# Kernel tuning notes

Measured on AMD Instinct MI355X. Metric: run time of the kernel, lower is better.

Reference implementation:

```python
import jax, jax.numpy as jnp
import numpy as np

FEATURE_SIZE = 1_000_000
CROSS_EMB = 16
NNZ = 819_200
BATCH = 16_384
NEG_SAMPLING_RATE = 1.0


def setup_inputs() -> dict:
    key = jax.random.key(0)
    k_ids, k_seg, k_lw, k_cw, k_b = jax.random.split(key, 5)
    ids = jax.random.randint(k_ids, (NNZ,), 0, FEATURE_SIZE, dtype=jnp.int64 if jax.config.jax_enable_x64 else jnp.int32).astype(jnp.int32)
    segment_ids = jnp.sort(jax.random.randint(k_seg, (NNZ,), 0, BATCH, dtype=jnp.int32))
    linear_bias = jax.random.normal(k_b, (1,), dtype=jnp.float32) * 1e-4
    linear_w = jax.random.normal(k_lw, (FEATURE_SIZE, 1), dtype=jnp.float32) * 1e-4
    cross_emb_w = jax.random.normal(k_cw, (FEATURE_SIZE, CROSS_EMB), dtype=jnp.float32) * 1e-4
    return {
        "ids": ids,
        "segment_ids": segment_ids,
        "batch_size": BATCH,
        "linear_bias": linear_bias,
        "linear_w": linear_w,
        "cross_emb_w": cross_emb_w,
    }


def reference(ids, segment_ids, batch_size, linear_bias, linear_w, cross_emb_w):
    # Embedding-bag (sum combiner) == segment_sum of gathered rows.
    # Partitioned-shard routing in the original is mathematically a single
    # global gather + segment_sum (shard partial sums add up to the same).
    lin_rows = linear_w[ids]                        # [N, 1]
    logits_wide = jax.ops.segment_sum(lin_rows, segment_ids, num_segments=batch_size)  # [B, 1]
    logits_linear = linear_bias + logits_wide

    cross_rows = cross_emb_w[ids]                   # [N, D]
    summed = jax.ops.segment_sum(cross_rows, segment_ids, num_segments=batch_size)     # [B, D]
    squared_summed = jnp.square(summed)
    summed_squared = jax.ops.segment_sum(jnp.square(cross_rows), segment_ids, num_segments=batch_size)
    # FM second-order interaction term
    logits_cross = 0.5 * jnp.sum(squared_summed - summed_squared, axis=1, keepdims=True)  # [B, 1]

    logits = logits_linear + logits_cross
    logits_adjusted = logits + jnp.log(jnp.float32(NEG_SAMPLING_RATE))
    probabilities = jax.nn.sigmoid(logits_adjusted)
    return (logits, logits_adjusted, probabilities)
```

## Files before the change

### kernel.cpp

```cpp
#include <hip/hip_runtime.h>
#include <math.h>


__global__ __launch_bounds__(256) void seg_starts_kernel(
    const int* __restrict__ segs, int* __restrict__ starts, int nnz, int batch)
{
    const int i = blockIdx.x * blockDim.x + threadIdx.x;
    if (i >= nnz) return;
    const int cur = segs[i];
    if (i == 0) {
        for (int b = 0; b <= cur; ++b) starts[b] = 0;
    } else {
        const int prev = segs[i - 1];
        for (int b = prev + 1; b <= cur; ++b) starts[b] = i;
    }
    if (i == nnz - 1) {
        for (int b = cur + 1; b <= batch; ++b) starts[b] = nnz;
    }
}

__global__ __launch_bounds__(256) void fm_fused_kernel(
    const int* __restrict__ ids,
    const int* __restrict__ starts,
    const float* __restrict__ bias,
    const float* __restrict__ lw,
    const float* __restrict__ cw,
    float* __restrict__ out,
    int batch)
{
    const int wave = threadIdx.x >> 6;
    const int wl   = threadIdx.x & 63;
    const int b    = blockIdx.x * 4 + wave;
    if (b >= batch) return;

    const int start = starts[b];
    const int end   = starts[b + 1];

    float sd[16];
    #pragma unroll
    for (int d = 0; d < 16; ++d) sd[d] = 0.f;
    float ssq = 0.f;
    float slin = 0.f;

    for (int i = start + wl; i < end; i += 64) {
        const int id = ids[i];
        const float* row = cw + ((size_t)id << 4);
        const float4 x0 = *reinterpret_cast<const float4*>(row);
        const float4 x1 = *reinterpret_cast<const float4*>(row + 4);
        const float4 x2 = *reinterpret_cast<const float4*>(row + 8);
        const float4 x3 = *reinterpret_cast<const float4*>(row + 12);
        slin += lw[id];
        sd[ 0] += x0.x; sd[ 1] += x0.y; sd[ 2] += x0.z; sd[ 3] += x0.w;
        sd[ 4] += x1.x; sd[ 5] += x1.y; sd[ 6] += x1.z; sd[ 7] += x1.w;
        sd[ 8] += x2.x; sd[ 9] += x2.y; sd[10] += x2.z; sd[11] += x2.w;
        sd[12] += x3.x; sd[13] += x3.y; sd[14] += x3.z; sd[15] += x3.w;
        ssq = fmaf(x0.x, x0.x, ssq); ssq = fmaf(x0.y, x0.y, ssq);
        ssq = fmaf(x0.z, x0.z, ssq); ssq = fmaf(x0.w, x0.w, ssq);
        ssq = fmaf(x1.x, x1.x, ssq); ssq = fmaf(x1.y, x1.y, ssq);
        ssq = fmaf(x1.z, x1.z, ssq); ssq = fmaf(x1.w, x1.w, ssq);
        ssq = fmaf(x2.x, x2.x, ssq); ssq = fmaf(x2.y, x2.y, ssq);
        ssq = fmaf(x2.z, x2.z, ssq); ssq = fmaf(x2.w, x2.w, ssq);
        ssq = fmaf(x3.x, x3.x, ssq); ssq = fmaf(x3.y, x3.y, ssq);
        ssq = fmaf(x3.w, x3.w, ssq); ssq = fmaf(x3.z, x3.z, ssq);
    }

    #pragma unroll
    for (int m = 1; m < 64; m <<= 1) {
        #pragma unroll
        for (int d = 0; d < 16; ++d) sd[d] += __shfl_xor(sd[d], m);
        ssq  += __shfl_xor(ssq,  m);
        slin += __shfl_xor(slin, m);
    }

    if (wl == 0) {
        float q = 0.f;
        #pragma unroll
        for (int d = 0; d < 16; ++d) q = fmaf(sd[d], sd[d], q);
        const float logit = bias[0] + slin + 0.5f * (q - ssq);
        const float adj   = logit;
        out[b]             = logit;
        out[batch + b]     = adj;
        out[2 * batch + b] = 1.0f / (1.0f + expf(-adj));
    }
}

extern "C" void kernel_launch(void* const* d_in, const int* in_sizes, int n_in,
                              void* d_out, int out_size, void* d_ws, size_t ws_size,
                              hipStream_t stream) {
    const int*   ids  = (const int*)d_in[0];
    const int*   segs = (const int*)d_in[1];
    const float* bias = (const float*)d_in[3];
    const float* lw   = (const float*)d_in[4];
    const float* cw   = (const float*)d_in[5];
    float*       out  = (float*)d_out;

    const int nnz   = in_sizes[0];
    const int batch = out_size / 3;

    int* starts = (int*)d_ws;

    seg_starts_kernel<<<(nnz + 255) / 256, 256, 0, stream>>>(segs, starts, nnz, batch);

    const int waves_per_block = 4;
    const int grid = (batch + waves_per_block - 1) / waves_per_block;
    fm_fused_kernel<<<grid, 256, 0, stream>>>(ids, starts, bias, lw, cw, out, batch);
}
```

Measured before the change: 125.0 us.

## Replace per-segment wave reduction with per-nnz segmented scan and atomics

Replaces the segment-starts plus one-wave-per-bag design with a thread-per-nonzero gather. A segmented inclusive scan using shuffle-up combines rows within a wave, and segment tails atomically add 18 partial sums into a zeroed workspace. A separate epilogue kernel then computes the logits and sigmoid. The goal is to avoid the load imbalance and idle lanes of waves assigned to short bags (about 50 nnz per bag across 64 lanes). In exchange it adds a third kernel launch, a workspace zero pass, global atomics, and 18 values times 6 shuffle steps per thread.

New measurement: 142.4 us. +13.9%, slower.

```diff
diff --git a/kernel.cpp b/kernel.cpp
--- a/kernel.cpp
+++ b/kernel.cpp
@@ -2,86 +2,86 @@
 #include <math.h>
 
 
-__global__ __launch_bounds__(256) void seg_starts_kernel(
-    const int* __restrict__ segs, int* __restrict__ starts, int nnz, int batch)
+#define WS_STRIDE 18
+
+__global__ __launch_bounds__(256) void zero_ws_kernel(float* __restrict__ ws, int n)
 {
-    const int i = blockIdx.x * blockDim.x + threadIdx.x;
-    if (i >= nnz) return;
-    const int cur = segs[i];
-    if (i == 0) {
-        for (int b = 0; b <= cur; ++b) starts[b] = 0;
-    } else {
-        const int prev = segs[i - 1];
-        for (int b = prev + 1; b <= cur; ++b) starts[b] = i;
-    }
-    if (i == nnz - 1) {
-        for (int b = cur + 1; b <= batch; ++b) starts[b] = nnz;
-    }
+    const int i = blockIdx.x * 256 + threadIdx.x;
+    if (i < n) ws[i] = 0.f;
 }
 
-__global__ __launch_bounds__(256) void fm_fused_kernel(
+__global__ __launch_bounds__(256) void fm_gather_kernel(
     const int* __restrict__ ids,
-    const int* __restrict__ starts,
-    const float* __restrict__ bias,
+    const int* __restrict__ segs,
     const float* __restrict__ lw,
     const float* __restrict__ cw,
-    float* __restrict__ out,
-    int batch)
+    float* __restrict__ ws,
+    int nnz)
 {
-    const int wave = threadIdx.x >> 6;
-    const int wl   = threadIdx.x & 63;
-    const int b    = blockIdx.x * 4 + wave;
-    if (b >= batch) return;
+    const int i    = blockIdx.x * 256 + threadIdx.x;
+    const int lane = threadIdx.x & 63;
 
-    const int start = starts[b];
-    const int end   = starts[b + 1];
+    int seg = -1;
+    float v[18];
+    #pragma unroll
+    for (int d = 0; d < 18; ++d) v[d] = 0.f;
 
-    float sd[16];
-    #pragma unroll
-    for (int d = 0; d < 16; ++d) sd[d] = 0.f;
-    float ssq = 0.f;
-    float slin = 0.f;
-
-    for (int i = start + wl; i < end; i += 64) {
+    if (i < nnz) {
+        seg = segs[i];
         const int id = ids[i];
         const float* row = cw + ((size_t)id << 4);
         const float4 x0 = *reinterpret_cast<const float4*>(row);
         const float4 x1 = *reinterpret_cast<const float4*>(row + 4);
         const float4 x2 = *reinterpret_cast<const float4*>(row + 8);
         const float4 x3 = *reinterpret_cast<const float4*>(row + 12);
-        slin += lw[id];
-        sd[ 0] += x0.x; sd[ 1] += x0.y; sd[ 2] += x0.z; sd[ 3] += x0.w;
-        sd[ 4] += x1.x; sd[ 5] += x1.y; sd[ 6] += x1.z; sd[ 7] += x1.w;
-        sd[ 8] += x2.x; sd[ 9] += x2.y; sd[10] += x2.z; sd[11] += x2.w;
-        sd[12] += x3.x; sd[13] += x3.y; sd[14] += x3.z; sd[15] += x3.w;
-        ssq = fmaf(x0.x, x0.x, ssq); ssq = fmaf(x0.y, x0.y, ssq);
-        ssq = fmaf(x0.z, x0.z, ssq); ssq = fmaf(x0.w, x0.w, ssq);
-        ssq = fmaf(x1.x, x1.x, ssq); ssq = fmaf(x1.y, x1.y, ssq);
-        ssq = fmaf(x1.z, x1.z, ssq); ssq = fmaf(x1.w, x1.w, ssq);
-        ssq = fmaf(x2.x, x2.x, ssq); ssq = fmaf(x2.y, x2.y, ssq);
-        ssq = fmaf(x2.z, x2.z, ssq); ssq = fmaf(x2.w, x2.w, ssq);
-        ssq = fmaf(x3.x, x3.x, ssq); ssq = fmaf(x3.y, x3.y, ssq);
-        ssq = fmaf(x3.w, x3.w, ssq); ssq = fmaf(x3.z, x3.z, ssq);
+        const float l  = lw[id];
+        v[ 0] = x0.x; v[ 1] = x0.y; v[ 2] = x0.z; v[ 3] = x0.w;
+        v[ 4] = x1.x; v[ 5] = x1.y; v[ 6] = x1.z; v[ 7] = x1.w;
+        v[ 8] = x2.x; v[ 9] = x2.y; v[10] = x2.z; v[11] = x2.w;
+        v[12] = x3.x; v[13] = x3.y; v[14] = x3.z; v[15] = x3.w;
+        float ssq = 0.f;
+        #pragma unroll
+        for (int d = 0; d < 16; ++d) ssq = fmaf(v[d], v[d], ssq);
+        v[16] = ssq;
+        v[17] = l;
     }
 
     #pragma unroll
-    for (int m = 1; m < 64; m <<= 1) {
+    for (int k = 1; k < 64; k <<= 1) {
+        const int oseg = __shfl_up(seg, k, 64);
+        const bool take = (lane >= k) && (oseg == seg);
         #pragma unroll
-        for (int d = 0; d < 16; ++d) sd[d] += __shfl_xor(sd[d], m);
-        ssq  += __shfl_xor(ssq,  m);
-        slin += __shfl_xor(slin, m);
+        for (int d = 0; d < 18; ++d) {
+            const float ov = __shfl_up(v[d], k, 64);
+            if (take) v[d] += ov;
+        }
     }
 
-    if (wl == 0) {
-        float q = 0.f;
+    const int nseg = __shfl_down(seg, 1, 64);
+    const bool tail = (lane == 63) || (nseg != seg);
+    if (tail && seg >= 0) {
+        float* dst = ws + (size_t)seg * WS_STRIDE;
         #pragma unroll
-        for (int d = 0; d < 16; ++d) q = fmaf(sd[d], sd[d], q);
-        const float logit = bias[0] + slin + 0.5f * (q - ssq);
-        const float adj   = logit;
-        out[b]             = logit;
-        out[batch + b]     = adj;
-        out[2 * batch + b] = 1.0f / (1.0f + expf(-adj));
+        for (int d = 0; d < 18; ++d) atomicAdd(dst + d, v[d]);
     }
+}
+
+__global__ __launch_bounds__(256) void fm_epilogue_kernel(
+    const float* __restrict__ ws,
+    const float* __restrict__ bias,
+    float* __restrict__ out,
+    int batch)
+{
+    const int b = blockIdx.x * 256 + threadIdx.x;
+    if (b >= batch) return;
+    const float* a = ws + (size_t)b * WS_STRIDE;
+    float q = 0.f;
+    #pragma unroll
+    for (int d = 0; d < 16; ++d) q = fmaf(a[d], a[d], q);
+    const float logit = bias[0] + a[17] + 0.5f * (q - a[16]);
+    out[b]             = logit;
+    out[batch + b]     = logit;
+    out[2 * batch + b] = 1.0f / (1.0f + expf(-logit));
 }
 
 extern "C" void kernel_launch(void* const* d_in, const int* in_sizes, int n_in,
@@ -97,11 +97,10 @@
     const int nnz   = in_sizes[0];
     const int batch = out_size / 3;
 
-    int* starts = (int*)d_ws;
+    float* ws = (float*)d_ws;
+    const int ws_n = batch * WS_STRIDE;
 
-    seg_starts_kernel<<<(nnz + 255) / 256, 256, 0, stream>>>(segs, starts, nnz, batch);
-
-    const int waves_per_block = 4;
-    const int grid = (batch + waves_per_block - 1) / waves_per_block;
-    fm_fused_kernel<<<grid, 256, 0, stream>>>(ids, starts, bias, lw, cw, out, batch);
+    zero_ws_kernel<<<(ws_n + 255) / 256, 256, 0, stream>>>(ws, ws_n);
+    fm_gather_kernel<<<(nnz + 255) / 256, 256, 0, stream>>>(ids, segs, lw, cw, ws, nnz);
+    fm_epilogue_kernel<<<(batch + 255) / 256, 256, 0, stream>>>(ws, bias, out, batch);
 }
```

## Split embedding rows across 4 lanes and shrink the wave reduction

Applied to the files above, without the earlier changes.

Each wave now handles 16 rows at a time, with four lanes sharing one 64-byte row and each loading a float4 slice. Two rows per lane are processed per iteration so more loads are in flight. The shuffle reduction drops from 16 components across 6 steps to 4 components across 4 steps plus a scalar reduction over 2 steps. Segments average about 50 rows, so the old layout left most lanes idle; the new mapping uses lanes better and gives each load four coalesced lanes.

After: 123.4 us. About the same (-1.3%).

```diff
diff --git a/kernel.cpp b/kernel.cpp
--- a/kernel.cpp
+++ b/kernel.cpp
@@ -36,51 +36,57 @@
     const int start = starts[b];
     const int end   = starts[b + 1];
 
-    float sd[16];
-    #pragma unroll
-    for (int d = 0; d < 16; ++d) sd[d] = 0.f;
-    float ssq = 0.f;
-    float slin = 0.f;
+    const int e = wl >> 2;
+    const int c = wl & 3;
 
-    for (int i = start + wl; i < end; i += 64) {
-        const int id = ids[i];
-        const float* row = cw + ((size_t)id << 4);
-        const float4 x0 = *reinterpret_cast<const float4*>(row);
-        const float4 x1 = *reinterpret_cast<const float4*>(row + 4);
-        const float4 x2 = *reinterpret_cast<const float4*>(row + 8);
-        const float4 x3 = *reinterpret_cast<const float4*>(row + 12);
-        slin += lw[id];
-        sd[ 0] += x0.x; sd[ 1] += x0.y; sd[ 2] += x0.z; sd[ 3] += x0.w;
-        sd[ 4] += x1.x; sd[ 5] += x1.y; sd[ 6] += x1.z; sd[ 7] += x1.w;
-        sd[ 8] += x2.x; sd[ 9] += x2.y; sd[10] += x2.z; sd[11] += x2.w;
-        sd[12] += x3.x; sd[13] += x3.y; sd[14] += x3.z; sd[15] += x3.w;
+    float4 sd = make_float4(0.f, 0.f, 0.f, 0.f);
+    float ssq = 0.f, slin = 0.f;
+
+    int i = start + e;
+    for (; i + 16 < end; i += 32) {
+        const int id0 = ids[i];
+        const int id1 = ids[i + 16];
+        const float4 x0 = *reinterpret_cast<const float4*>(cw + ((size_t)id0 << 4) + (c << 2));
+        const float4 x1 = *reinterpret_cast<const float4*>(cw + ((size_t)id1 << 4) + (c << 2));
+        if (c == 0) slin += lw[id0] + lw[id1];
+        sd.x += x0.x; sd.y += x0.y; sd.z += x0.z; sd.w += x0.w;
+        sd.x += x1.x; sd.y += x1.y; sd.z += x1.z; sd.w += x1.w;
         ssq = fmaf(x0.x, x0.x, ssq); ssq = fmaf(x0.y, x0.y, ssq);
         ssq = fmaf(x0.z, x0.z, ssq); ssq = fmaf(x0.w, x0.w, ssq);
         ssq = fmaf(x1.x, x1.x, ssq); ssq = fmaf(x1.y, x1.y, ssq);
         ssq = fmaf(x1.z, x1.z, ssq); ssq = fmaf(x1.w, x1.w, ssq);
-        ssq = fmaf(x2.x, x2.x, ssq); ssq = fmaf(x2.y, x2.y, ssq);
-        ssq = fmaf(x2.z, x2.z, ssq); ssq = fmaf(x2.w, x2.w, ssq);
-        ssq = fmaf(x3.x, x3.x, ssq); ssq = fmaf(x3.y, x3.y, ssq);
-        ssq = fmaf(x3.w, x3.w, ssq); ssq = fmaf(x3.z, x3.z, ssq);
+    }
+    if (i < end) {
+        const int id0 = ids[i];
+        const float4 x0 = *reinterpret_cast<const float4*>(cw + ((size_t)id0 << 4) + (c << 2));
+        if (c == 0) slin += lw[id0];
+        sd.x += x0.x; sd.y += x0.y; sd.z += x0.z; sd.w += x0.w;
+        ssq = fmaf(x0.x, x0.x, ssq); ssq = fmaf(x0.y, x0.y, ssq);
+        ssq = fmaf(x0.z, x0.z, ssq); ssq = fmaf(x0.w, x0.w, ssq);
     }
 
     #pragma unroll
-    for (int m = 1; m < 64; m <<= 1) {
-        #pragma unroll
-        for (int d = 0; d < 16; ++d) sd[d] += __shfl_xor(sd[d], m);
+    for (int m = 4; m <= 32; m <<= 1) {
+        sd.x += __shfl_xor(sd.x, m);
+        sd.y += __shfl_xor(sd.y, m);
+        sd.z += __shfl_xor(sd.z, m);
+        sd.w += __shfl_xor(sd.w, m);
+        ssq  += __shfl_xor(ssq,  m);
+        slin += __shfl_xor(slin, m);
+    }
+    float q = sd.x*sd.x + sd.y*sd.y + sd.z*sd.z + sd.w*sd.w;
+    #pragma unroll
+    for (int m = 1; m <= 2; m <<= 1) {
+        q    += __shfl_xor(q,    m);
         ssq  += __shfl_xor(ssq,  m);
         slin += __shfl_xor(slin, m);
     }
 
     if (wl == 0) {
-        float q = 0.f;
-        #pragma unroll
-        for (int d = 0; d < 16; ++d) q = fmaf(sd[d], sd[d], q);
         const float logit = bias[0] + slin + 0.5f * (q - ssq);
-        const float adj   = logit;
         out[b]             = logit;
-        out[batch + b]     = adj;
-        out[2 * batch + b] = 1.0f / (1.0f + expf(-adj));
+        out[batch + b]     = logit;
+        out[2 * batch + b] = 1.0f / (1.0f + expf(-logit));
     }
 }
 
```
